# Kernel optimization log

Hardware: AMD Instinct MI355X
Metric: run time of the kernel (lower is better)

## Reference

```python
import jax, jax.numpy as jnp
import numpy as np

TEMPERATURE = 0.1
EPS = 1e-8  # torch cosine_similarity default eps


def _similarity_matrix(left, right):
    # C[i, j] = cosine_similarity(left[i], right[j]) with torch-style eps clamp
    ln = jnp.linalg.norm(left, axis=-1)   # [B]
    rn = jnp.linalg.norm(right, axis=-1)  # [B]
    dots = left @ right.T                 # [B, B]
    denom = jnp.maximum(ln[:, None] * rn[None, :], EPS)
    cos = dots / denom
    # Original builds only the strict upper triangle + diagonal of C, then
    # mirrors the upper triangle: S = triu(C, 1) + diag(C) + triu(C, 1).T
    upper = jnp.triu(cos, k=1)
    return upper + jnp.diag(jnp.diag(cos)) + upper.T


def reference(left_features, right_features):
    sims = _similarity_matrix(left_features, right_features) / TEMPERATURE
    # cross_entropy(sims, eye) == mean_i( -log_softmax(sims)[i, i] )
    logp = jax.nn.log_softmax(sims, axis=-1)
    return -jnp.mean(jnp.diagonal(logp))


def setup_inputs() -> dict:
    key = jax.random.key(0)
    k1, k2 = jax.random.split(key)
    B, D = 4096, 1024
    return {
        "left_features": jax.random.normal(k1, (B, D), dtype=jnp.float32),
        "right_features": jax.random.normal(k2, (B, D), dtype=jnp.float32),
    }
```

## Files before the change

### kernel.cpp

```cpp
#include <hip/hip_runtime.h>

typedef unsigned short u16;
typedef __bf16 bf16x8 __attribute__((ext_vector_type(8)));
typedef float f32x4 __attribute__((ext_vector_type(4)));

#define B_DIM 4096
#define D_DIM 1024
#define TT    32

#define GLOAD_LDS16(g, l)                                            \
    __builtin_amdgcn_global_load_lds(                                \
        (const __attribute__((address_space(1))) void*)(g),          \
        (__attribute__((address_space(3))) void*)(l), 16, 0, 0)

__device__ inline u16 f2bf(float f) {
    union { float f; unsigned u; } x; x.f = f;
    unsigned u = x.u;
    return (u16)((u + 0x7fffu + ((u >> 16) & 1u)) >> 16);
}

__device__ inline float wave_reduce_sum(float v) {
    #pragma unroll
    for (int off = 32; off > 0; off >>= 1) v += __shfl_down(v, off);
    return v;
}

__global__ __launch_bounds__(256) void norm_convert_kernel(
        const float* __restrict__ L, const float* __restrict__ R,
        u16* __restrict__ Lbf, u16* __restrict__ Rbf,
        float* __restrict__ ln, float* __restrict__ rn) {
    int b = blockIdx.x;
    const float* in; u16* outb; float* nout; int row;
    if (b < B_DIM) { in = L; outb = Lbf; nout = ln; row = b; }
    else           { in = R; outb = Rbf; nout = rn; row = b - B_DIM; }

    const float4* r4 = reinterpret_cast<const float4*>(in + (size_t)row * D_DIM);
    ushort4* o4 = reinterpret_cast<ushort4*>(outb + (size_t)row * D_DIM);
    float ss = 0.f;
    for (int c = threadIdx.x; c < (D_DIM >> 2); c += blockDim.x) {
        float4 v = r4[c];
        ss += v.x * v.x + v.y * v.y + v.z * v.z + v.w * v.w;
        ushort4 o;
        o.x = f2bf(v.x); o.y = f2bf(v.y); o.z = f2bf(v.z); o.w = f2bf(v.w);
        o4[c] = o;
    }
    __shared__ float red[4];
    float w = wave_reduce_sum(ss);
    if ((threadIdx.x & 63) == 0) red[threadIdx.x >> 6] = w;
    __syncthreads();
    if (threadIdx.x == 0)
        nout[row] = sqrtf(red[0] + red[1] + red[2] + red[3]);
}

__global__ __launch_bounds__(256) void gemm_fused_kernel(
        const u16* __restrict__ Lbf, const u16* __restrict__ Rbf,
        const float* __restrict__ ln, const float* __restrict__ rn,
        float* __restrict__ rowsum, float* __restrict__ diag) {
    __shared__ __align__(16) u16 Ls[128 * 64];
    __shared__ __align__(16) u16 Rs[128 * 64];

    int b = (int)blockIdx.x;
    int ti = 0;
    while (b >= TT - ti) { b -= TT - ti; ++ti; }
    const int tj = ti + b;
    const int brow = ti * 128;
    const int bcol = tj * 128;
    const bool diagblk = (ti == tj);

    const int tid  = threadIdx.x;
    const int lane = tid & 63;
    const int wave = tid >> 6;
    const int wr   = wave >> 1;
    const int wc   = wave & 1;
    const int fr   = lane & 15;

    const int l8 = lane >> 3;
    const int c8 = lane & 7;
    size_t gA[4], gB[4];
    u16 *lA[4], *lB[4];
    #pragma unroll
    for (int s = 0; s < 4; ++s) {
        int row = (wave * 4 + s) * 8 + l8;
        int chunk = c8 ^ (row & 7);
        gA[s] = (size_t)(brow + row) * D_DIM + chunk * 8;
        gB[s] = (size_t)(bcol + row) * D_DIM + chunk * 8;
        lA[s] = Ls + (wave * 4 + s) * 512;
        lB[s] = Rs + (wave * 4 + s) * 512;
    }

    f32x4 acc[4][4] = {};

    for (int k0 = 0; k0 < D_DIM; k0 += 64) {
        #pragma unroll
        for (int s = 0; s < 4; ++s) {
            GLOAD_LDS16(Lbf + gA[s] + k0, lA[s]);
            GLOAD_LDS16(Rbf + gB[s] + k0, lB[s]);
        }
        __syncthreads();

        #pragma unroll
        for (int kk = 0; kk < 2; ++kk) {
            bf16x8 af[4], bfr[4];
            #pragma unroll
            for (int m = 0; m < 4; ++m) {
                int row = wr * 64 + m * 16 + fr;
                int cs = ((kk << 2) | (lane >> 4)) ^ (row & 7);
                af[m] = *reinterpret_cast<const bf16x8*>(&Ls[row * 64 + cs * 8]);
            }
            #pragma unroll
            for (int n = 0; n < 4; ++n) {
                int row = wc * 64 + n * 16 + fr;
                int cs = ((kk << 2) | (lane >> 4)) ^ (row & 7);
                bfr[n] = *reinterpret_cast<const bf16x8*>(&Rs[row * 64 + cs * 8]);
            }
            #pragma unroll
            for (int m = 0; m < 4; ++m)
                #pragma unroll
                for (int n = 0; n < 4; ++n)
                    acc[m][n] = __builtin_amdgcn_mfma_f32_16x16x32_bf16(
                        af[m], bfr[n], acc[m][n], 0, 0, 0);
        }
        __syncthreads();
    }

    const int fcol  = lane & 15;
    const int frow0 = (lane >> 4) * 4;

    float rnj[4];
    #pragma unroll
    for (int n = 0; n < 4; ++n)
        rnj[n] = rn[bcol + wc * 64 + n * 16 + fcol];

    float colacc[4] = {0.f, 0.f, 0.f, 0.f};

    #pragma unroll
    for (int m = 0; m < 4; ++m) {
        #pragma unroll
        for (int r = 0; r < 4; ++r) {
            const int i = brow + wr * 64 + m * 16 + frow0 + r;
            const float lni = ln[i];
            float rowacc = 0.f;
            #pragma unroll
            for (int n = 0; n < 4; ++n) {
                const int j = bcol + wc * 64 + n * 16 + fcol;
                const float denom = fmaxf(lni * rnj[n], 1e-8f);
                const float v = acc[m][n][r] * 10.0f / denom;
                if (diagblk && i == j) diag[i] = v;
                const float e = __expf(v);
                if (i <= j) rowacc += e;
                if (i < j)  colacc[n] += e;
            }
            rowacc += __shfl_xor(rowacc, 1);
            rowacc += __shfl_xor(rowacc, 2);
            rowacc += __shfl_xor(rowacc, 4);
            rowacc += __shfl_xor(rowacc, 8);
            if (fcol == 0) atomicAdd(&rowsum[i], rowacc);
        }
    }
    #pragma unroll
    for (int n = 0; n < 4; ++n) {
        float c = colacc[n];
        c += __shfl_xor(c, 16);
        c += __shfl_xor(c, 32);
        if (lane < 16) {
            const int j = bcol + wc * 64 + n * 16 + fcol;
            atomicAdd(&rowsum[j], c);
        }
    }
}

__global__ __launch_bounds__(256) void final_loss_kernel(
        const float* __restrict__ rowsum, const float* __restrict__ diag,
        float* __restrict__ out) {
    float s = 0.f;
    for (int i = threadIdx.x; i < B_DIM; i += 256)
        s += logf(rowsum[i]) - diag[i];
    __shared__ float red[4];
    float w = wave_reduce_sum(s);
    if ((threadIdx.x & 63) == 0) red[threadIdx.x >> 6] = w;
    __syncthreads();
    if (threadIdx.x == 0)
        out[0] = (red[0] + red[1] + red[2] + red[3]) / (float)B_DIM;
}

extern "C" void kernel_launch(void* const* d_in, const int* in_sizes, int n_in,
                              void* d_out, int out_size, void* d_ws, size_t ws_size,
                              hipStream_t stream) {
    const float* L = (const float*)d_in[0];
    const float* R = (const float*)d_in[1];

    char* ws = (char*)d_ws;
    size_t o = 0;
    u16* Lbf   = (u16*)(ws + o);   o += (size_t)B_DIM * D_DIM * sizeof(u16);
    u16* Rbf   = (u16*)(ws + o);   o += (size_t)B_DIM * D_DIM * sizeof(u16);
    float* ln  = (float*)(ws + o); o += (size_t)B_DIM * sizeof(float);
    float* rn  = (float*)(ws + o); o += (size_t)B_DIM * sizeof(float);
    float* rs  = (float*)(ws + o); o += (size_t)B_DIM * sizeof(float);
    float* dg  = (float*)(ws + o); o += (size_t)B_DIM * sizeof(float);

    hipMemsetAsync(rs, 0, B_DIM * sizeof(float), stream);

    norm_convert_kernel<<<2 * B_DIM, 256, 0, stream>>>(L, R, Lbf, Rbf, ln, rn);

    const int nblocks = TT * (TT + 1) / 2;
    gemm_fused_kernel<<<nblocks, 256, 0, stream>>>(Lbf, Rbf, ln, rn, rs, dg);

    final_loss_kernel<<<1, 256, 0, stream>>>(rs, dg, (float*)d_out);
}
```

Before: 141.3 us.

## Double-buffer GEMM LDS tiles, use one wave per row in norm kernel

The GEMM main loop now uses two LDS buffers. The next K-slice is issued with async global-to-LDS loads while the current slice runs through MFMA, which needs only one barrier per iteration instead of two. The norm/convert kernel now assigns one row per wave and reduces with shuffles only, dropping the shared-memory reduction and block barrier. The final loss kernel runs 1024 threads. Doubling LDS to 64KB per block may lower occupancy.

```diff
diff --git a/kernel.cpp b/kernel.cpp
--- a/kernel.cpp
+++ b/kernel.cpp
@@ -29,35 +29,35 @@
         const float* __restrict__ L, const float* __restrict__ R,
         u16* __restrict__ Lbf, u16* __restrict__ Rbf,
         float* __restrict__ ln, float* __restrict__ rn) {
-    int b = blockIdx.x;
+    const int wave = threadIdx.x >> 6;
+    const int lane = threadIdx.x & 63;
+    int g = blockIdx.x * 4 + wave;
     const float* in; u16* outb; float* nout; int row;
-    if (b < B_DIM) { in = L; outb = Lbf; nout = ln; row = b; }
-    else           { in = R; outb = Rbf; nout = rn; row = b - B_DIM; }
+    if (g < B_DIM) { in = L; outb = Lbf; nout = ln; row = g; }
+    else           { in = R; outb = Rbf; nout = rn; row = g - B_DIM; }
 
     const float4* r4 = reinterpret_cast<const float4*>(in + (size_t)row * D_DIM);
     ushort4* o4 = reinterpret_cast<ushort4*>(outb + (size_t)row * D_DIM);
     float ss = 0.f;
-    for (int c = threadIdx.x; c < (D_DIM >> 2); c += blockDim.x) {
-        float4 v = r4[c];
+    #pragma unroll
+    for (int c = 0; c < 4; ++c) {
+        float4 v = r4[lane + 64 * c];
         ss += v.x * v.x + v.y * v.y + v.z * v.z + v.w * v.w;
         ushort4 o;
         o.x = f2bf(v.x); o.y = f2bf(v.y); o.z = f2bf(v.z); o.w = f2bf(v.w);
-        o4[c] = o;
-    }
-    __shared__ float red[4];
-    float w = wave_reduce_sum(ss);
-    if ((threadIdx.x & 63) == 0) red[threadIdx.x >> 6] = w;
-    __syncthreads();
-    if (threadIdx.x == 0)
-        nout[row] = sqrtf(red[0] + red[1] + red[2] + red[3]);
+        o4[lane + 64 * c] = o;
+    }
+    #pragma unroll
+    for (int off = 32; off > 0; off >>= 1) ss += __shfl_xor(ss, off);
+    if (lane == 0) nout[row] = sqrtf(ss);
 }
 
 __global__ __launch_bounds__(256) void gemm_fused_kernel(
         const u16* __restrict__ Lbf, const u16* __restrict__ Rbf,
         const float* __restrict__ ln, const float* __restrict__ rn,
         float* __restrict__ rowsum, float* __restrict__ diag) {
-    __shared__ __align__(16) u16 Ls[128 * 64];
-    __shared__ __align__(16) u16 Rs[128 * 64];
+    __shared__ __align__(16) u16 Ls[2][128 * 64];
+    __shared__ __align__(16) u16 Rs[2][128 * 64];
 
     int b = (int)blockIdx.x;
     int ti = 0;
@@ -77,51 +77,66 @@
     const int l8 = lane >> 3;
     const int c8 = lane & 7;
     size_t gA[4], gB[4];
-    u16 *lA[4], *lB[4];
+    int ldsOff[4];
     #pragma unroll
     for (int s = 0; s < 4; ++s) {
         int row = (wave * 4 + s) * 8 + l8;
         int chunk = c8 ^ (row & 7);
         gA[s] = (size_t)(brow + row) * D_DIM + chunk * 8;
         gB[s] = (size_t)(bcol + row) * D_DIM + chunk * 8;
-        lA[s] = Ls + (wave * 4 + s) * 512;
-        lB[s] = Rs + (wave * 4 + s) * 512;
-    }
+        ldsOff[s] = (wave * 4 + s) * 512;
+    }
+
+#define STAGE(buf, k0)                                               \
+    do {                                                             \
+        _Pragma("unroll")                                            \
+        for (int s = 0; s < 4; ++s) {                                \
+            GLOAD_LDS16(Lbf + gA[s] + (k0), &Ls[buf][ldsOff[s]]);    \
+            GLOAD_LDS16(Rbf + gB[s] + (k0), &Rs[buf][ldsOff[s]]);    \
+        }                                                            \
+    } while (0)
 
     f32x4 acc[4][4] = {};
 
-    for (int k0 = 0; k0 < D_DIM; k0 += 64) {
-        #pragma unroll
-        for (int s = 0; s < 4; ++s) {
-            GLOAD_LDS16(Lbf + gA[s] + k0, lA[s]);
-            GLOAD_LDS16(Rbf + gB[s] + k0, lB[s]);
-        }
+#define COMPUTE(buf)                                                  \
+    do {                                                              \
+        _Pragma("unroll")                                             \
+        for (int kk = 0; kk < 2; ++kk) {                              \
+            bf16x8 af[4], bfr[4];                                     \
+            _Pragma("unroll")                                         \
+            for (int m = 0; m < 4; ++m) {                             \
+                int row = wr * 64 + m * 16 + fr;                      \
+                int cs = ((kk << 2) | (lane >> 4)) ^ (row & 7);       \
+                af[m] = *reinterpret_cast<const bf16x8*>(             \
+                    &Ls[buf][row * 64 + cs * 8]);                     \
+            }                                                         \
+            _Pragma("unroll")                                         \
+            for (int n = 0; n < 4; ++n) {                             \
+                int row = wc * 64 + n * 16 + fr;                      \
+                int cs = ((kk << 2) | (lane >> 4)) ^ (row & 7);       \
+                bfr[n] = *reinterpret_cast<const bf16x8*>(            \
+                    &Rs[buf][row * 64 + cs * 8]);                     \
+            }                                                         \
+            _Pragma("unroll")                                         \
+            for (int m = 0; m < 4; ++m)                               \
+                _Pragma("unroll")                                     \
+                for (int n = 0; n < 4; ++n)                           \
+                    acc[m][n] = __builtin_amdgcn_mfma_f32_16x16x32_bf16( \
+                        af[m], bfr[n], acc[m][n], 0, 0, 0);           \
+        }                                                             \
+    } while (0)
+
+    STAGE(0, 0);
+    __syncthreads();
+
+    int cur = 0;
+    for (int t = 0; t < 15; ++t) {
+        STAGE(cur ^ 1, (t + 1) * 64);
+        COMPUTE(cur);
         __syncthreads();
-
-        #pragma unroll
-        for (int kk = 0; kk < 2; ++kk) {
-            bf16x8 af[4], bfr[4];
-            #pragma unroll
-            for (int m = 0; m < 4; ++m) {
-                int row = wr * 64 + m * 16 + fr;
-                int cs = ((kk << 2) | (lane >> 4)) ^ (row & 7);
-                af[m] = *reinterpret_cast<const bf16x8*>(&Ls[row * 64 + cs * 8]);
-            }
-            #pragma unroll
-            for (int n = 0; n < 4; ++n) {
-                int row = wc * 64 + n * 16 + fr;
-                int cs = ((kk << 2) | (lane >> 4)) ^ (row & 7);
-                bfr[n] = *reinterpret_cast<const bf16x8*>(&Rs[row * 64 + cs * 8]);
-            }
-            #pragma unroll
-            for (int m = 0; m < 4; ++m)
-                #pragma unroll
-                for (int n = 0; n < 4; ++n)
-                    acc[m][n] = __builtin_amdgcn_mfma_f32_16x16x32_bf16(
-                        af[m], bfr[n], acc[m][n], 0, 0, 0);
-        }
-        __syncthreads();
-    }
+        cur ^= 1;
+    }
+    COMPUTE(cur);
 
     const int fcol  = lane & 15;
     const int frow0 = (lane >> 4) * 4;
@@ -167,20 +182,26 @@
             atomicAdd(&rowsum[j], c);
         }
     }
-}
-
-__global__ __launch_bounds__(256) void final_loss_kernel(
+#undef STAGE
+#undef COMPUTE
+}
+
+__global__ __launch_bounds__(1024) void final_loss_kernel(
         const float* __restrict__ rowsum, const float* __restrict__ diag,
         float* __restrict__ out) {
     float s = 0.f;
-    for (int i = threadIdx.x; i < B_DIM; i += 256)
+    for (int i = threadIdx.x; i < B_DIM; i += 1024)
         s += logf(rowsum[i]) - diag[i];
-    __shared__ float red[4];
+    __shared__ float red[16];
     float w = wave_reduce_sum(s);
     if ((threadIdx.x & 63) == 0) red[threadIdx.x >> 6] = w;
     __syncthreads();
-    if (threadIdx.x == 0)
-        out[0] = (red[0] + red[1] + red[2] + red[3]) / (float)B_DIM;
+    if (threadIdx.x == 0) {
+        float tot = 0.f;
+        #pragma unroll
+        for (int k = 0; k < 16; ++k) tot += red[k];
+        out[0] = tot / (float)B_DIM;
+    }
 }
 
 extern "C" void kernel_launch(void* const* d_in, const int* in_sizes, int n_in,
@@ -200,10 +221,10 @@
 
     hipMemsetAsync(rs, 0, B_DIM * sizeof(float), stream);
 
-    norm_convert_kernel<<<2 * B_DIM, 256, 0, stream>>>(L, R, Lbf, Rbf, ln, rn);
+    norm_convert_kernel<<<2 * B_DIM / 4, 256, 0, stream>>>(L, R, Lbf, Rbf, ln, rn);
 
     const int nblocks = TT * (TT + 1) / 2;
     gemm_fused_kernel<<<nblocks, 256, 0, stream>>>(Lbf, Rbf, ln, rn, rs, dg);
 
-    final_loss_kernel<<<1, 256, 0, stream>>>(rs, dg, (float*)d_out);
-}
+    final_loss_kernel<<<1, 1024, 0, stream>>>(rs, dg, (float*)d_out);
+}
```

After: 138.5 us. 1.02x faster.
